# Kernel optimization log

Hardware: AMD Instinct MI355X
Metric: run time of the kernel (lower is better)

Reference implementation:

```python
import jax, jax.numpy as jnp
import numpy as np
from jax import lax

# dims
B, H, W, C = 32, 64, 64, 256
FEATURES, HEADS, NQ = 256, 8, 2
K, STRIDE, PAD = 3, 2, 1
HD = FEATURES // HEADS  # head dim = 32


def setup_inputs() -> dict:
    key = jax.random.key(0)
    ks = jax.random.split(key, 7)
    x = jax.random.normal(ks[0], (B, H, W, C), jnp.float32)
    # learned shared queries: truncated normal * sqrt(1/head_dim)
    query = jax.random.truncated_normal(ks[1], -2.0, 2.0, (NQ, FEATURES), jnp.float32) * np.float32(np.sqrt(1.0 / HD))
    Wk = jax.random.normal(ks[2], (C, FEATURES), jnp.float32) * np.float32(np.sqrt(1.0 / C))  # lecun
    Wv = jax.random.normal(ks[3], (C, FEATURES), jnp.float32) * np.float32(np.sqrt(1.0 / C))
    rpe_bias = jax.random.truncated_normal(ks[4], -2.0, 2.0, (K * K, NQ * HEADS), jnp.float32) * np.float32(0.02)
    attn_scale_w = jax.random.normal(ks[5], (K * K, NQ * HEADS), jnp.float32) * np.float32(0.02)
    Wo = jax.random.normal(ks[6], (FEATURES, FEATURES), jnp.float32) * np.float32(np.sqrt(1.0 / FEATURES))
    return {"x": x, "query": query, "Wk": Wk, "Wv": Wv,
            "rpe_bias": rpe_bias, "attn_scale_w": attn_scale_w, "Wo": Wo}


def _qna_forward(x, query, Wk, Wv, rpe_bias, attn_scale_w, Wo):
    # --- queries: reshape to [NQ, HEADS, HD], unit-normalize per head, depth-scale ---
    q = query.reshape(NQ, HEADS, HD)
    q = q / (jnp.linalg.norm(q, axis=-1, keepdims=True) + 1e-6)
    q = q / jnp.sqrt(HD).astype(q.dtype)

    # --- fused QK: (q Wk^T) applied to x, never materializing per-window keys ---
    Wk_r = Wk.reshape(C, HEADS, HD)
    qWk = jnp.einsum('qHd,DHd->DqH', q, Wk_r)              # [C, NQ, HEADS]
    cost = jnp.einsum('bijD,DqH->bijqH', x, qWk)            # [B, H, W, NQ, HEADS]
    cost_exp = jnp.exp(cost - lax.stop_gradient(jnp.max(cost)))  # global shift, cancels in softmax

    # --- values ---
    v = jnp.einsum('bijD,DF->bijF', x, Wv)                  # [B, H, W, FEATURES]
    v_cost_exp = cost_exp[..., None] * v.reshape(B, H, W, 1, HEADS, HD)
    v_cost_exp = v_cost_exp.reshape(B, H, W, NQ * FEATURES)

    # --- relative position bias + per-offset query mixing scale ---
    rpe = rpe_bias.reshape(K, K, 1, NQ * HEADS)
    rpe_exp = jnp.exp(rpe - lax.stop_gradient(jnp.max(rpe)))  # shift cancels (appears in num & den)
    scale = attn_scale_w.reshape(K, K, 1, NQ * HEADS)
    num_kernel = jnp.repeat(rpe_exp * scale, HD, axis=-1)   # [K, K, 1, NQ*FEATURES]

    # numerator: windowed sum of exp(cost)*v weighted by exp(rpe)*scale (depthwise conv)
    num = lax.conv_general_dilated(
        v_cost_exp, num_kernel, window_strides=(STRIDE, STRIDE),
        padding=((PAD, PAD), (PAD, PAD)), feature_group_count=NQ * FEATURES,
        dimension_numbers=('NHWC', 'HWIO', 'NHWC'))
    # denominator: windowed sum of exp(cost) weighted by exp(rpe)
    den = lax.conv_general_dilated(
        cost_exp.reshape(B, H, W, NQ * HEADS), rpe_exp, window_strides=(STRIDE, STRIDE),
        padding=((PAD, PAD), (PAD, PAD)), feature_group_count=NQ * HEADS,
        dimension_numbers=('NHWC', 'HWIO', 'NHWC'))
    ho, wo = num.shape[1], num.shape[2]

    out = num.reshape(B, ho, wo, NQ, HEADS, HD) / den.reshape(B, ho, wo, NQ, HEADS, 1)
    out = out.sum(axis=3).reshape(B, ho, wo, FEATURES)      # combine queries
    return jnp.einsum('bijF,FO->bijO', out, Wo)             # output projection


def reference(x, query, Wk, Wv, rpe_bias, attn_scale_w, Wo):
    return _qna_forward(x, query, Wk, Wv, rpe_bias, attn_scale_w, Wo)
```

## Files before the change

### kernel.cpp

```cpp
#include <hip/hip_runtime.h>
#include <math.h>

typedef __attribute__((ext_vector_type(8))) short bf16x8;
typedef __attribute__((ext_vector_type(4))) float floatx4;

static __device__ __forceinline__ short f2bf(float f) {
    union { float f; unsigned u; } a; a.f = f;
    unsigned r = a.u + 0x7fffu + ((a.u >> 16) & 1u);
    return (short)(r >> 16);
}
static __device__ __forceinline__ float bf2f(short s) {
    union { unsigned u; float f; } c; c.u = ((unsigned)(unsigned short)s) << 16;
    return c.f;
}

__global__ __launch_bounds__(256) void prep_kernel(
    const float* __restrict__ query,
    const float* __restrict__ Wk,
    const float* __restrict__ rpe_bias,
    const float* __restrict__ attn_scale_w,
    const float* __restrict__ Wv,
    const float* __restrict__ Wo,
    float* __restrict__ rpe_exp,
    float* __restrict__ rpe_scale,
    short* __restrict__ Bq,
    short* __restrict__ Wvh,
    short* __restrict__ Bo)
{
    __shared__ float qn[16 * 33];
    __shared__ float Wt[16][260];
    __shared__ float qwk_s[16][17];
    int tid = threadIdx.x, bb = blockIdx.x;

    for (int i = tid; i < 512; i += 256) {
        int qq  = i >> 8;
        int rem = i & 255;
        int h   = rem >> 5;
        int d   = rem & 31;
        qn[((qq << 3) + h) * 33 + d] = query[i];
    }
    for (int i = tid; i < 16 * 256; i += 256)
        Wt[i >> 8][i & 255] = Wk[bb * 16 * 256 + i];
    __syncthreads();
    if (tid < 16) {
        float s = 0.f;
        #pragma unroll
        for (int d = 0; d < 32; ++d) { float t = qn[tid * 33 + d]; s += t * t; }
        float inv = 1.0f / ((sqrtf(s) + 1e-6f) * sqrtf(32.0f));
        #pragma unroll
        for (int d = 0; d < 32; ++d) qn[tid * 33 + d] *= inv;
    }
    __syncthreads();

    int g  = tid & 15;
    int Dl = tid >> 4;
    int h2 = g & 7;
    float acc = 0.f;
    #pragma unroll
    for (int d = 0; d < 32; ++d)
        acc += qn[g * 33 + d] * Wt[Dl][h2 * 32 + d];
    qwk_s[Dl][g] = acc;
    __syncthreads();

    {
        int kl = tid >> 4, gg = tid & 15;
        int k  = bb * 16 + kl;
        int kc = k >> 5, q5 = k & 31, qd = q5 >> 3, j = q5 & 7;
        int lane = qd * 16 + gg;
        Bq[kc * 512 + lane * 8 + j] = f2bf(qwk_s[kl][gg]);
    }

    for (int kl = 0; kl < 16; ++kl) {
        int k  = bb * 16 + kl;
        int kc = k >> 5, q5 = k & 31, qd = q5 >> 3, j = q5 & 7;
        int n  = tid;
        int gg = n & 15;
        int lane = qd * 16 + gg;
        float vv = Wv[k * 256 + n];
        float vo = Wo[k * 256 + n];
        int nt  = n >> 4;
        Wvh[nt * 4096 + kc * 512 + lane * 8 + j] = f2bf(vv);
        Bo[nt * 4096 + kc * 512 + lane * 8 + j]  = f2bf(vo);
    }

    if (bb == 0 && tid < 144) {
        float r = expf(rpe_bias[tid]);
        rpe_exp[tid]   = r;
        rpe_scale[tid] = r * attn_scale_w[tid];
    }
}

#define XROW 264
#define CESROW 19
__global__ __launch_bounds__(512) void fused_kernel(
    const float* __restrict__ x,
    const float* __restrict__ rpe_exp,
    const float* __restrict__ rpe_scale,
    const short* __restrict__ Bq,
    const short* __restrict__ Wvh,
    const short* __restrict__ Bo,
    float* __restrict__ out)
{
    __shared__ short Xw[112 * XROW];
    __shared__ __align__(16) unsigned char pool[112 * CESROW * 4];
    __shared__ float wcoefs[8][9][16];
    __shared__ float invden[16][16];

    float* ces    = (float*)pool;
    short* out_tr = (short*)pool;

    int tid  = threadIdx.x;
    int lane = tid & 63, wv = tid >> 6;
    int m16  = lane & 15, quad = lane >> 4;

    int blk0 = blockIdx.x;
    int blk  = ((blk0 & 7) << 8) | (blk0 >> 3);
    int b   = blk >> 6;
    int io  = (blk >> 1) & 31;
    int hf  = blk & 1;
    int i0  = io * 2 - 1;
    int jbase = hf * 32 - 1;

    #pragma unroll
    for (int i = 0; i < 7; ++i) {
        int it  = tid + i * 512;
        int row = it >> 5;
        int l   = it & 31;
        int ky  = row / 34;
        int jloc = row - ky * 34;
        int ii = i0 + ky, jj = jbase + jloc;
        bool valid = (ky < 3) && (jloc < 33) &&
                     ((unsigned)ii < 64u) && ((unsigned)jj < 64u);
        bf16x8 s;
        if (valid) {
            const float* xp = x + ((size_t)(((b << 6) + ii) << 6) + jj) * 256 + l * 8;
            float4 f0 = *(const float4*)xp;
            float4 f1 = *(const float4*)(xp + 4);
            s[0] = f2bf(f0.x); s[1] = f2bf(f0.y); s[2] = f2bf(f0.z); s[3] = f2bf(f0.w);
            s[4] = f2bf(f1.x); s[5] = f2bf(f1.y); s[6] = f2bf(f1.z); s[7] = f2bf(f1.w);
        } else {
            #pragma unroll
            for (int j = 0; j < 8; ++j) s[j] = 0;
        }
        *(bf16x8*)&Xw[row * XROW + l * 8] = s;
    }
    __syncthreads();

    bf16x8 Bv0[8], Bv1[8];
    {
        const short* bv = Wvh + (2 * wv) * 4096 + lane * 8;
        #pragma unroll
        for (int kc = 0; kc < 8; ++kc) {
            Bv0[kc] = *(const bf16x8*)(bv + kc * 512);
            Bv1[kc] = *(const bf16x8*)(bv + 4096 + kc * 512);
        }
    }

    if (wv < 7) {
        floatx4 accc = (floatx4){0.f, 0.f, 0.f, 0.f};
        const short* bq   = Bq + lane * 8;
        const short* xrow = &Xw[(wv * 16 + m16) * XROW + quad * 8];
        #pragma unroll
        for (int kc = 0; kc < 8; ++kc) {
            bf16x8 a = *(const bf16x8*)(xrow + kc * 32);
            accc = __builtin_amdgcn_mfma_f32_16x16x32_bf16(
                       a, *(const bf16x8*)(bq + kc * 512), accc, 0, 0, 0);
        }
        #pragma unroll
        for (int r = 0; r < 4; ++r) {
            int p = wv * 16 + quad * 4 + r;
            int ky = p / 34, jloc = p - ky * 34;
            int ii = i0 + ky, jj = jbase + jloc;
            bool valid = (ky < 3) && (jloc < 33) &&
                         ((unsigned)ii < 64u) && ((unsigned)jj < 64u);
            ces[p * CESROW + m16] = valid ? expf(accc[r]) : 0.f;
        }
    }

    for (int m = 0; m < 7; ++m) {
        floatx4 a0 = (floatx4){0.f, 0.f, 0.f, 0.f};
        floatx4 a1 = (floatx4){0.f, 0.f, 0.f, 0.f};
        const short* xrow = &Xw[(m * 16 + m16) * XROW + quad * 8];
        #pragma unroll
        for (int kc = 0; kc < 8; ++kc) {
            bf16x8 af = *(const bf16x8*)(xrow + kc * 32);
            a0 = __builtin_amdgcn_mfma_f32_16x16x32_bf16(af, Bv0[kc], a0, 0, 0, 0);
            a1 = __builtin_amdgcn_mfma_f32_16x16x32_bf16(af, Bv1[kc], a1, 0, 0, 0);
        }
        __syncthreads();
        #pragma unroll
        for (int r = 0; r < 4; ++r) {
            Xw[(m * 16 + quad * 4 + r) * XROW + wv * 32 + m16]      = f2bf(a0[r]);
            Xw[(m * 16 + quad * 4 + r) * XROW + wv * 32 + 16 + m16] = f2bf(a1[r]);
        }
    }

    __syncthreads();
    if (tid < 256) {
        int op = tid >> 4, g = tid & 15;
        float den = 0.f;
        #pragma unroll
        for (int w = 0; w < 9; ++w) {
            int ky = w / 3, kx = w - ky * 3;
            int row = ky * 34 + 2 * op + kx;
            den = fmaf(rpe_exp[w * 16 + g], ces[row * CESROW + g], den);
        }
        invden[op][g] = 1.0f / den;
    }
    __syncthreads();

    for (int it = tid; it < 1152; it += 512) {
        int op = it / 72, r = it - op * 72;
        int w = r >> 3, h = r & 7;
        int ky = w / 3, kx = w - ky * 3;
        int row = ky * 34 + 2 * op + kx;
        wcoefs[h][w][op] =
            ces[row * CESROW + h]     * rpe_scale[w * 16 + h]     * invden[op][h] +
            ces[row * CESROW + 8 + h] * rpe_scale[w * 16 + 8 + h] * invden[op][8 + h];
    }
    __syncthreads();

    {
        int op = tid >> 5;
        int nc = tid & 31;
        int n0 = nc * 8;
        int h  = nc >> 2;
        float wcv[9];
        #pragma unroll
        for (int w = 0; w < 9; ++w) wcv[w] = wcoefs[h][w][op];

        float o[8];
        #pragma unroll
        for (int j = 0; j < 8; ++j) o[j] = 0.f;
        #pragma unroll
        for (int w = 0; w < 9; ++w) {
            int ky = w / 3, kx = w - ky * 3;
            int row = ky * 34 + 2 * op + kx;
            bf16x8 vv = *(const bf16x8*)&Xw[row * XROW + n0];
            #pragma unroll
            for (int j = 0; j < 8; ++j)
                o[j] = fmaf(wcv[w], bf2f(vv[j]), o[j]);
        }
        bf16x8 ob;
        #pragma unroll
        for (int j = 0; j < 8; ++j) ob[j] = f2bf(o[j]);
        *(bf16x8*)&out_tr[op * XROW + n0] = ob;
    }
    __syncthreads();

    {
        floatx4 acc0 = (floatx4){0.f, 0.f, 0.f, 0.f};
        floatx4 acc1 = (floatx4){0.f, 0.f, 0.f, 0.f};
        int nt0 = wv * 2;
        const short* bp = Bo + nt0 * 4096 + lane * 8;
        #pragma unroll
        for (int kc = 0; kc < 8; ++kc) {
            bf16x8 a  = *(const bf16x8*)&out_tr[m16 * XROW + kc * 32 + quad * 8];
            bf16x8 b0 = *(const bf16x8*)(bp + kc * 512);
            bf16x8 b1 = *(const bf16x8*)(bp + 4096 + kc * 512);
            acc0 = __builtin_amdgcn_mfma_f32_16x16x32_bf16(a, b0, acc0, 0, 0, 0);
            acc1 = __builtin_amdgcn_mfma_f32_16x16x32_bf16(a, b1, acc1, 0, 0, 0);
        }
        size_t op0 = (size_t)blk * 16;
        #pragma unroll
        for (int r = 0; r < 4; ++r) {
            out[(op0 + quad * 4 + r) * 256 + nt0 * 16 + m16]       = acc0[r];
            out[(op0 + quad * 4 + r) * 256 + (nt0 + 1) * 16 + m16] = acc1[r];
        }
    }
}

extern "C" void kernel_launch(void* const* d_in, const int* in_sizes, int n_in,
                              void* d_out, int out_size, void* d_ws, size_t ws_size,
                              hipStream_t stream)
{
    const float* x     = (const float*)d_in[0];
    const float* query = (const float*)d_in[1];
    const float* Wk    = (const float*)d_in[2];
    const float* Wv    = (const float*)d_in[3];
    const float* rpe   = (const float*)d_in[4];
    const float* asw   = (const float*)d_in[5];
    const float* Wo    = (const float*)d_in[6];
    float* out = (float*)d_out;

    float* ws        = (float*)d_ws;
    float* rpe_exp   = ws;
    float* rpe_scale = ws + 144;
    short* Bq        = (short*)(ws + 288);
    short* Wvh       = (short*)(ws + 288 + 2048);
    short* Bo        = (short*)(ws + 288 + 2048 + 32768);

    prep_kernel<<<dim3(16), dim3(256), 0, stream>>>(query, Wk, rpe, asw, Wv, Wo,
                                                    rpe_exp, rpe_scale, Bq, Wvh, Bo);
    fused_kernel<<<dim3(2048), dim3(512), 0, stream>>>(x, rpe_exp, rpe_scale,
                                                       Bq, Wvh, Bo, out);
}
```

Before: 257.4 us.

## Swizzle LDS tiles into MFMA fragment layout and fold cost GEMM into value loop

Replaces the padded row-major shared-memory tile with an XOR-swizzled layout that matches the MFMA A-fragment order, for X, V and the output staging buffer. The goal is fewer LDS bank conflicts and simpler addressing. The cost GEMM is moved into the value-projection loop, so each wave issues its cost MFMAs while reading the same A fragment. The kernel also gains a minimum-occupancy launch bound of 4, which may constrain register allocation.

```diff
diff --git a/kernel.cpp b/kernel.cpp
--- a/kernel.cpp
+++ b/kernel.cpp
@@ -12,6 +12,10 @@
 static __device__ __forceinline__ float bf2f(short s) {
     union { unsigned u; float f; } c; c.u = ((unsigned)(unsigned short)s) << 16;
     return c.f;
+}
+
+static __device__ __forceinline__ int xa_idx(int m, int kc, int quad, int m16) {
+    return m * 4096 + kc * 512 + (quad * 16 + (m16 ^ ((kc * 4 + quad) & 15))) * 8;
 }
 
 __global__ __launch_bounds__(256) void prep_kernel(
@@ -90,9 +94,8 @@
     }
 }
 
-#define XROW 264
 #define CESROW 19
-__global__ __launch_bounds__(512) void fused_kernel(
+__global__ __launch_bounds__(512, 4) void fused_kernel(
     const float* __restrict__ x,
     const float* __restrict__ rpe_exp,
     const float* __restrict__ rpe_scale,
@@ -101,7 +104,7 @@
     const short* __restrict__ Bo,
     float* __restrict__ out)
 {
-    __shared__ short Xw[112 * XROW];
+    __shared__ __align__(16) short Xw[7 * 4096];
     __shared__ __align__(16) unsigned char pool[112 * CESROW * 4];
     __shared__ float wcoefs[8][9][16];
     __shared__ float invden[16][16];
@@ -142,7 +145,8 @@
             #pragma unroll
             for (int j = 0; j < 8; ++j) s[j] = 0;
         }
-        *(bf16x8*)&Xw[row * XROW + l * 8] = s;
+        int dst = xa_idx(row >> 4, l >> 2, l & 3, row & 15);
+        *(bf16x8*)&Xw[dst] = s;
     }
     __syncthreads();
 
@@ -156,42 +160,39 @@
         }
     }
 
-    if (wv < 7) {
-        floatx4 accc = (floatx4){0.f, 0.f, 0.f, 0.f};
-        const short* bq   = Bq + lane * 8;
-        const short* xrow = &Xw[(wv * 16 + m16) * XROW + quad * 8];
-        #pragma unroll
-        for (int kc = 0; kc < 8; ++kc) {
-            bf16x8 a = *(const bf16x8*)(xrow + kc * 32);
-            accc = __builtin_amdgcn_mfma_f32_16x16x32_bf16(
-                       a, *(const bf16x8*)(bq + kc * 512), accc, 0, 0, 0);
-        }
-        #pragma unroll
-        for (int r = 0; r < 4; ++r) {
-            int p = wv * 16 + quad * 4 + r;
-            int ky = p / 34, jloc = p - ky * 34;
-            int ii = i0 + ky, jj = jbase + jloc;
-            bool valid = (ky < 3) && (jloc < 33) &&
-                         ((unsigned)ii < 64u) && ((unsigned)jj < 64u);
-            ces[p * CESROW + m16] = valid ? expf(accc[r]) : 0.f;
-        }
-    }
-
     for (int m = 0; m < 7; ++m) {
         floatx4 a0 = (floatx4){0.f, 0.f, 0.f, 0.f};
         floatx4 a1 = (floatx4){0.f, 0.f, 0.f, 0.f};
-        const short* xrow = &Xw[(m * 16 + m16) * XROW + quad * 8];
+        floatx4 accc = (floatx4){0.f, 0.f, 0.f, 0.f};
+        bool docost = (wv == m);
+        const short* bq = Bq + lane * 8;
         #pragma unroll
         for (int kc = 0; kc < 8; ++kc) {
-            bf16x8 af = *(const bf16x8*)(xrow + kc * 32);
+            bf16x8 af = *(const bf16x8*)&Xw[xa_idx(m, kc, quad, m16)];
             a0 = __builtin_amdgcn_mfma_f32_16x16x32_bf16(af, Bv0[kc], a0, 0, 0, 0);
             a1 = __builtin_amdgcn_mfma_f32_16x16x32_bf16(af, Bv1[kc], a1, 0, 0, 0);
+            if (docost)
+                accc = __builtin_amdgcn_mfma_f32_16x16x32_bf16(
+                           af, *(const bf16x8*)(bq + kc * 512), accc, 0, 0, 0);
+        }
+        if (docost) {
+            #pragma unroll
+            for (int r = 0; r < 4; ++r) {
+                int p = wv * 16 + quad * 4 + r;
+                int ky = p / 34, jloc = p - ky * 34;
+                int ii = i0 + ky, jj = jbase + jloc;
+                bool valid = (ky < 3) && (jloc < 33) &&
+                             ((unsigned)ii < 64u) && ((unsigned)jj < 64u);
+                ces[p * CESROW + m16] = valid ? expf(accc[r]) : 0.f;
+            }
         }
         __syncthreads();
         #pragma unroll
         for (int r = 0; r < 4; ++r) {
-            Xw[(m * 16 + quad * 4 + r) * XROW + wv * 32 + m16]      = f2bf(a0[r]);
-            Xw[(m * 16 + quad * 4 + r) * XROW + wv * 32 + 16 + m16] = f2bf(a1[r]);
+            int lr = quad * 4 + r;
+            short* vrow = &Xw[m * 4096 + lr * 256];
+            vrow[(wv * 32 + m16) ^ (quad << 4)]      = f2bf(a0[r]);
+            vrow[(wv * 32 + 16 + m16) ^ (quad << 4)] = f2bf(a1[r]);
         }
     }
 
@@ -223,7 +224,6 @@
     {
         int op = tid >> 5;
         int nc = tid & 31;
-        int n0 = nc * 8;
         int h  = nc >> 2;
         float wcv[9];
         #pragma unroll
@@ -235,8 +235,10 @@
         #pragma unroll
         for (int w = 0; w < 9; ++w) {
             int ky = w / 3, kx = w - ky * 3;
-            int row = ky * 34 + 2 * op + kx;
-            bf16x8 vv = *(const bf16x8*)&Xw[row * XROW + n0];
+            int vr = ky * 34 + 2 * op + kx;
+            int lr = vr & 15;
+            int ncs = nc ^ ((lr >> 2) << 1);
+            bf16x8 vv = *(const bf16x8*)&Xw[(vr >> 4) * 4096 + lr * 256 + ncs * 8];
             #pragma unroll
             for (int j = 0; j < 8; ++j)
                 o[j] = fmaf(wcv[w], bf2f(vv[j]), o[j]);
@@ -244,7 +246,8 @@
         bf16x8 ob;
         #pragma unroll
         for (int j = 0; j < 8; ++j) ob[j] = f2bf(o[j]);
-        *(bf16x8*)&out_tr[op * XROW + n0] = ob;
+        *(bf16x8*)&out_tr[(nc >> 2) * 512 +
+                          ((nc & 3) * 16 + (op ^ (nc & 15))) * 8] = ob;
     }
     __syncthreads();
 
@@ -255,7 +258,7 @@
         const short* bp = Bo + nt0 * 4096 + lane * 8;
         #pragma unroll
         for (int kc = 0; kc < 8; ++kc) {
-            bf16x8 a  = *(const bf16x8*)&out_tr[m16 * XROW + kc * 32 + quad * 8];
+            bf16x8 a = *(const bf16x8*)&out_tr[xa_idx(0, kc, quad, m16)];
             bf16x8 b0 = *(const bf16x8*)(bp + kc * 512);
             bf16x8 b1 = *(const bf16x8*)(bp + 4096 + kc * 512);
             acc0 = __builtin_amdgcn_mfma_f32_16x16x32_bf16(a, b0, acc0, 0, 0, 0);
```

Result: slower. 278.0 us (+8.0%).
